# Kernel optimization log

Measured on AMD Instinct MI355X. Metric: run time of the kernel, lower is better.

The kernel has to match this reference:

```python
import jax, jax.numpy as jnp
import numpy as np

SPATIAL = 8  # spatial_size


def setup_inputs() -> dict:
    key = jax.random.key(0)
    k1, k2 = jax.random.split(key)
    B, C, T, H, W = 8, 1, 16, 500, 500
    inp = jax.random.normal(k1, (B, C, T, H, W), dtype=jnp.float32)
    stdv = 1.0 / np.sqrt(T)  # matches reset_parameters scaling
    weight = jax.random.uniform(k2, (T, 4, 4), dtype=jnp.float32, minval=-stdv, maxval=stdv)
    return {"input": inp, "weight": weight, "pad_h": 512, "pad_w": 512,
            "n_patch_h": 127, "n_patch_w": 127}


def reference(input, weight, pad_h, pad_w, n_patch_h, n_patch_w):
    B, C, T, H, W = input.shape
    step = weight.shape[1]  # spatial_size // 2 (overlapping)
    s = SPATIAL

    # zero-pad bottom/right to the padded frame size
    x = jnp.pad(input, ((0, 0), (0, 0), (0, 0), (0, pad_h - H), (0, pad_w - W)))

    # weight.repeat(B, C, 1, n_patch_h+1, n_patch_w+1): tile step-blocks over frame;
    # broadcast over (B, C) instead of materializing the full repeat.
    w_tiled = jnp.tile(weight, (1, n_patch_h + 1, n_patch_w + 1))  # (T, pad_h, pad_w)

    # masked multiply + temporal sum -> coded snapshot (B, C, pad_h, pad_w)
    output = jnp.einsum('bcthw,thw->bchw', x, w_tiled)

    # overlapping patch extraction: unfold(2, s, step).unfold(3, s, step)
    hh = (jnp.arange(n_patch_h) * step)[:, None] + jnp.arange(s)  # (nph, s)
    ww = (jnp.arange(n_patch_w) * step)[:, None] + jnp.arange(s)  # (npw, s)
    patches = output[:, :, hh[:, None, :, None], ww[None, :, None, :]]  # (B,C,nph,npw,s,s)

    # permute(0,1,2,3,5,4) then flatten to (B, C*nph*npw, s*s)
    patches = jnp.swapaxes(patches, -1, -2)
    patches = patches.reshape(B, -1, s * s)

    return patches, output[:, :, :H, :W]
```

## Files before the change

kernel.cpp:

```cpp
#include <hip/hip_runtime.h>

#define B_DIM 8
#define T_DIM 16
#define H_IN 500
#define W_IN 500
#define NPH 127
#define NPW 127
#define LSTR 516
#define NT 512
#define BANDS 32
#define ROWS 16
#define XROWS 20

typedef float f4 __attribute__((ext_vector_type(4)));

__global__ __launch_bounds__(NT) void k_band(const float* __restrict__ in,
                                             const float* __restrict__ wgt,
                                             float* __restrict__ patches,
                                             float* __restrict__ crop) {
    __shared__ float lds[XROWS * LSTR];
    __shared__ f4 wlds[T_DIM * 4];
    int tid = threadIdx.x;
    if (tid < T_DIM * 4) wlds[tid] = reinterpret_cast<const f4*>(wgt)[tid];

    int orig = blockIdx.x;
    int b = orig & 7;
    int q = orig >> 3;
    __syncthreads();

    #pragma unroll
    for (int k = 0; k < 5; ++k) {
        int e = tid + k * NT;
        int r = e >> 7;
        int c = (e & 127) * 4;
        int h = q * ROWS + r;
        f4 acc = {0.f, 0.f, 0.f, 0.f};
        if (h < H_IN && c < W_IN) {
            const float* base = in + (size_t)b * T_DIM * (H_IN * W_IN) + h * W_IN + c;
            int hr = h & 3;
            #pragma unroll
            for (int t = 0; t < T_DIM; ++t)
                acc += *reinterpret_cast<const f4*>(base + (size_t)t * (H_IN * W_IN))
                       * wlds[t * 4 + hr];
            if (r < ROWS)
                *reinterpret_cast<f4*>(crop + ((size_t)b * H_IN + h) * W_IN + c) = acc;
        }
        *reinterpret_cast<f4*>(&lds[r * LSTR + c]) = acc;
    }
    __syncthreads();

    f4* pbase = reinterpret_cast<f4*>(patches)
              + ((size_t)b * NPH + (size_t)4 * q) * NPW * 16;
    int nsub = (q == BANDS - 1) ? 3 : 4;
    for (int sub = 0; sub < nsub; ++sub) {
        f4* dst = pbase + (size_t)sub * NPW * 16;
        for (int e4 = tid; e4 < NPW * 16; e4 += NT) {
            int i0 = (e4 & 1) * 4;
            int j  = (e4 >> 1) & 7;
            int pw = e4 >> 4;
            int col = pw * 4 + j;
            int r0 = sub * 4 + i0;
            f4 v;
            v.x = lds[(r0 + 0) * LSTR + col];
            v.y = lds[(r0 + 1) * LSTR + col];
            v.z = lds[(r0 + 2) * LSTR + col];
            v.w = lds[(r0 + 3) * LSTR + col];
            dst[e4] = v;
        }
    }
}

extern "C" void kernel_launch(void* const* d_in, const int* in_sizes, int n_in,
                              void* d_out, int out_size, void* d_ws, size_t ws_size,
                              hipStream_t stream) {
    const float* in  = (const float*)d_in[0];
    const float* wgt = (const float*)d_in[1];
    float* out     = (float*)d_out;
    float* patches = out;
    float* crop    = out + (size_t)B_DIM * NPH * NPW * 64;

    k_band<<<B_DIM * BANDS, NT, 0, stream>>>(in, wgt, patches, crop);
}
```

Baseline: 34.13 us.

## Drop halo rows; split boundary patch rows across neighboring bands

Each block now computes only its own 16 rows instead of 20, so the 4-row halo that re-read all 16 time slices from global memory is gone. The patch row that straddles two bands is written half by each band: the top half comes from the current band's last 4 rows and the bottom half from the next band's first 4 rows, using strided partial f4 stores. This removes redundant input reads and compute, at the cost of less coalesced stores for the boundary patch rows.

```diff
diff --git a/kernel.cpp b/kernel.cpp
--- a/kernel.cpp
+++ b/kernel.cpp
@@ -10,7 +10,6 @@
 #define NT 512
 #define BANDS 32
 #define ROWS 16
-#define XROWS 20
 
 typedef float f4 __attribute__((ext_vector_type(4)));
 
@@ -18,7 +17,7 @@
                                              const float* __restrict__ wgt,
                                              float* __restrict__ patches,
                                              float* __restrict__ crop) {
-    __shared__ float lds[XROWS * LSTR];
+    __shared__ float lds[ROWS * LSTR];
     __shared__ f4 wlds[T_DIM * 4];
     int tid = threadIdx.x;
     if (tid < T_DIM * 4) wlds[tid] = reinterpret_cast<const f4*>(wgt)[tid];
@@ -29,7 +28,7 @@
     __syncthreads();
 
     #pragma unroll
-    for (int k = 0; k < 5; ++k) {
+    for (int k = 0; k < 4; ++k) {
         int e = tid + k * NT;
         int r = e >> 7;
         int c = (e & 127) * 4;
@@ -42,8 +41,7 @@
             for (int t = 0; t < T_DIM; ++t)
                 acc += *reinterpret_cast<const f4*>(base + (size_t)t * (H_IN * W_IN))
                        * wlds[t * 4 + hr];
-            if (r < ROWS)
-                *reinterpret_cast<f4*>(crop + ((size_t)b * H_IN + h) * W_IN + c) = acc;
+            *reinterpret_cast<f4*>(crop + ((size_t)b * H_IN + h) * W_IN + c) = acc;
         }
         *reinterpret_cast<f4*>(&lds[r * LSTR + c]) = acc;
     }
@@ -51,8 +49,8 @@
 
     f4* pbase = reinterpret_cast<f4*>(patches)
               + ((size_t)b * NPH + (size_t)4 * q) * NPW * 16;
-    int nsub = (q == BANDS - 1) ? 3 : 4;
-    for (int sub = 0; sub < nsub; ++sub) {
+    #pragma unroll
+    for (int sub = 0; sub < 3; ++sub) {
         f4* dst = pbase + (size_t)sub * NPW * 16;
         for (int e4 = tid; e4 < NPW * 16; e4 += NT) {
             int i0 = (e4 & 1) * 4;
@@ -68,6 +66,35 @@
             dst[e4] = v;
         }
     }
+    if (q < BANDS - 1) {
+        f4* dst = pbase + (size_t)3 * NPW * 16;
+        for (int e = tid; e < NPW * 8; e += NT) {
+            int j  = e & 7;
+            int pw = e >> 3;
+            int col = pw * 4 + j;
+            f4 v;
+            v.x = lds[12 * LSTR + col];
+            v.y = lds[13 * LSTR + col];
+            v.z = lds[14 * LSTR + col];
+            v.w = lds[15 * LSTR + col];
+            dst[pw * 16 + j * 2] = v;
+        }
+    }
+    if (q > 0) {
+        f4* dst = reinterpret_cast<f4*>(patches)
+                + ((size_t)b * NPH + (size_t)(4 * q - 1)) * NPW * 16;
+        for (int e = tid; e < NPW * 8; e += NT) {
+            int j  = e & 7;
+            int pw = e >> 3;
+            int col = pw * 4 + j;
+            f4 v;
+            v.x = lds[0 * LSTR + col];
+            v.y = lds[1 * LSTR + col];
+            v.z = lds[2 * LSTR + col];
+            v.w = lds[3 * LSTR + col];
+            dst[pw * 16 + j * 2 + 1] = v;
+        }
+    }
 }
 
 extern "C" void kernel_launch(void* const* d_in, const int* in_sizes, int n_in,
```

Measured after the change: 30.18 us. -11.6%, faster.
